# Performance work log

Measured on AMD Instinct MI355X. Metric: run time of the kernel, lower is better.

The kernel has to match this reference:

```python
import jax, jax.numpy as jnp
import numpy as np

HEAD_CHOICES = [8, 10, 12]
MAX_HEADS = 12
HEAD_DIM = 64
MAX_REL_POS = 14
SCALE = HEAD_DIM ** -0.5


def _rel_indices(N):
    # AutoFormer RelativePosition2D_super index computation (static, numpy).
    L = N - 1                      # remove cls token
    s = int(L ** 0.5)              # patches per row
    r = np.arange(L)
    dv = r[None, :] // s - r[:, None] // s
    dh = r[None, :] % s - r[:, None] % s
    iv = np.clip(dv, -MAX_REL_POS, MAX_REL_POS) + MAX_REL_POS + 1
    ih = np.clip(dh, -MAX_REL_POS, MAX_REL_POS) + MAX_REL_POS + 1
    iv = np.pad(iv, ((1, 0), (1, 0)))  # cls token row/col -> index 0
    ih = np.pad(ih, ((1, 0), (1, 0)))
    return jnp.asarray(iv), jnp.asarray(ih)


def setup_inputs() -> dict:
    key = jax.random.key(0)
    ks = jax.random.split(key, 6)
    B, N = 16, 577
    T = 2 * MAX_REL_POS + 2  # 30
    x = jax.random.normal(ks[0], (B, N, 3 * MAX_HEADS * HEAD_DIM), dtype=jnp.float32)
    weights = jax.nn.softmax(jax.random.normal(ks[1], (len(HEAD_CHOICES),), dtype=jnp.float32))
    rel_k_table_v = jax.random.normal(ks[2], (T, HEAD_DIM), dtype=jnp.float32) * 0.02
    rel_k_table_h = jax.random.normal(ks[3], (T, HEAD_DIM), dtype=jnp.float32) * 0.02
    rel_v_table_v = jax.random.normal(ks[4], (T, HEAD_DIM), dtype=jnp.float32) * 0.02
    rel_v_table_h = jax.random.normal(ks[5], (T, HEAD_DIM), dtype=jnp.float32) * 0.02
    return dict(x=x, weights=weights,
                rel_k_table_v=rel_k_table_v, rel_k_table_h=rel_k_table_h,
                rel_v_table_v=rel_v_table_v, rel_v_table_h=rel_v_table_h)


def reference(x, weights, rel_k_table_v, rel_k_table_h, rel_v_table_v, rel_v_table_h):
    B, N, _ = x.shape
    # [3, B, H, N, D]
    qkv = x.reshape(B, N, 3, MAX_HEADS, HEAD_DIM).transpose(2, 0, 3, 1, 4)
    # Mixture over head-count choices: slicing first c heads, scaling by w[i],
    # padding to max_heads, and summing == per-head weight sum_i w[i]*[h < c_i].
    head_mask = jnp.asarray(np.array([[1.0 if h < c else 0.0 for h in range(MAX_HEADS)]
                                      for c in HEAD_CHOICES]), dtype=x.dtype)  # [C, H]
    w_head = weights @ head_mask  # [H]
    w4 = w_head[None, :, None, None]
    q = qkv[0] * w4
    k = qkv[1] * w4
    v = qkv[2] * w4
    # content attention + relative-position K bias
    attn = jnp.einsum('bhnd,bhmd->bhnm', q, k) * SCALE
    iv, ih = _rel_indices(N)
    rel_k = rel_k_table_v[iv] + rel_k_table_h[ih]  # [N, N, D]
    attn = attn + jnp.einsum('bhnd,nmd->bhnm', q, rel_k) * SCALE
    attn = jax.nn.softmax(attn, axis=-1)  # attn_drop has p=0 (eval)
    out = jnp.einsum('bhnm,bhmd->bhnd', attn, v)
    rel_v = rel_v_table_v[iv] + rel_v_table_h[ih]  # [N, N, D]
    out = out + jnp.einsum('bhnm,nmd->bhnd', attn, rel_v)
    return out.transpose(0, 2, 1, 3).reshape(B, N, MAX_HEADS * HEAD_DIM)
```

## Files before the change

kernel.cpp:

```cpp
#include <hip/hip_runtime.h>

typedef short bf16x8_t __attribute__((ext_vector_type(8)));
typedef float f32x4_t __attribute__((ext_vector_type(4)));

#define NTOK 577
#define QPAD 640
#define MPAD 608
#define NSTEP 19

__device__ __forceinline__ unsigned short f2bf(float f) {
  unsigned u = __builtin_bit_cast(unsigned, f);
  u += 0x7FFFu + ((u >> 16) & 1u);
  return (unsigned short)(u >> 16);
}
__device__ __forceinline__ float headw(const float* wts, int h) {
  float w0 = wts[0], w1 = wts[1], w2 = wts[2];
  return (h < 8) ? (w0 + w1 + w2) : ((h < 10) ? (w1 + w2) : w2);
}
__device__ __forceinline__ unsigned rangemask(int lo, int hi) {
  lo = lo < 0 ? 0 : lo; hi = hi > 32 ? 32 : hi;
  if (hi <= lo) return 0u;
  unsigned mh = (hi >= 32) ? 0xFFFFFFFFu : ((1u << hi) - 1u);
  unsigned ml = (1u << lo) - 1u;
  return mh & ~ml;
}

extern "C" __global__ __launch_bounds__(256) void prep_x(
    const float* __restrict__ x, const float* __restrict__ wts,
    unsigned short* __restrict__ qbf, unsigned short* __restrict__ kbf,
    unsigned short* __restrict__ vbf) {
  __shared__ unsigned short t_s[64][72];
  const int tid = threadIdx.x;
  const int n0 = blockIdx.x * 64, h = blockIdx.y, b = blockIdx.z;
  const float w = headw(wts, h);
  const float qs = w * w * 0.125f;
  const float* xb = x + (size_t)(b * NTOK) * 2304 + h * 64;
  unsigned short* qo = qbf + ((size_t)(b * 12 + h)) * QPAD * 64;
  unsigned short* ko = kbf + ((size_t)(b * 12 + h)) * QPAD * 64;
  for (int p = 0; p < 4; ++p) {
    int idx = p * 256 + tid;
    int row = idx >> 4, c4 = idx & 15;
    int n = n0 + row;
    float4 vq = {0,0,0,0}, vk = {0,0,0,0}, vv = {0,0,0,0};
    if (n < NTOK) {
      const float* rp = xb + (size_t)n * 2304 + c4 * 4;
      vq = *(const float4*)rp;
      vk = *(const float4*)(rp + 768);
      vv = *(const float4*)(rp + 1536);
    }
    ushort4 oq, ok;
    oq.x = f2bf(vq.x * qs); oq.y = f2bf(vq.y * qs); oq.z = f2bf(vq.z * qs); oq.w = f2bf(vq.w * qs);
    ok.x = f2bf(vk.x); ok.y = f2bf(vk.y); ok.z = f2bf(vk.z); ok.w = f2bf(vk.w);
    *(ushort4*)(qo + (size_t)(n0 + row) * 64 + c4 * 4) = oq;
    *(ushort4*)(ko + (size_t)(n0 + row) * 64 + c4 * 4) = ok;
    t_s[c4 * 4 + 0][row] = f2bf(vv.x);
    t_s[c4 * 4 + 1][row] = f2bf(vv.y);
    t_s[c4 * 4 + 2][row] = f2bf(vv.z);
    t_s[c4 * 4 + 3][row] = f2bf(vv.w);
  }
  __syncthreads();
  for (int p = 0; p < 2; ++p) {
    int c = p * 256 + tid;
    int d = c >> 3, n8 = c & 7;
    bf16x8_t val = *(const bf16x8_t*)&t_s[d][n8 * 8];
    *(bf16x8_t*)(vbf + ((size_t)(b * 12 + h) * 64 + d) * QPAD + n0 + n8 * 8) = val;
  }
}

extern "C" __global__ __launch_bounds__(256) void prep_tab(
    const float* __restrict__ wts,
    const float* __restrict__ tkv, const float* __restrict__ tkh,
    const float* __restrict__ tvv, const float* __restrict__ tvh,
    unsigned short* __restrict__ tkb, unsigned short* __restrict__ tvb) {
  int tid = threadIdx.x, bx = blockIdx.x;
  if (bx < 48) {
    int cid = bx * 256 + tid;
    int d4 = cid & 15, t = (cid >> 4) & 31, tb = (cid >> 9) & 1, h = cid >> 10;
    float s = 1.f / headw(wts, h);
    const float* src = tb ? tkh : tkv;
    float4 v = {0,0,0,0};
    if (t < 30) v = *(const float4*)(src + t * 64 + d4 * 4);
    ushort4 o;
    o.x = f2bf(v.x * s); o.y = f2bf(v.y * s); o.z = f2bf(v.z * s); o.w = f2bf(v.w * s);
    *(ushort4*)(tkb + (((size_t)(h * 2 + tb)) * 32 + t) * 64 + d4 * 4) = o;
  } else {
    for (int i = 0; i < 16; ++i) {
      int id = tid * 16 + i;
      int t = id & 31, d = (id >> 5) & 63, tb = id >> 11;
      const float* src = tb ? tvh : tvv;
      tvb[id] = (t < 30) ? f2bf(src[t * 64 + d]) : (unsigned short)0;
    }
  }
}

struct __align__(16) SMem {
  float qg_s[2][64][25];
  unsigned gmask_s[2][NSTEP][25];
  float l_s[64];
  union {
    struct { float qv_t[2][64][30]; } pro;
    struct {
      unsigned short k_s[32][72];
      unsigned short v_sT[64][40];
      unsigned short P_s[64][40];
    } loop;
    struct { float sv_f[2][64][30]; } epi;
  } u;
};

extern "C" __global__ __launch_bounds__(256, 5) void hma_kernel(
    const unsigned short* __restrict__ qbf, const unsigned short* __restrict__ kbf,
    const unsigned short* __restrict__ vbf, const unsigned short* __restrict__ tkb,
    const unsigned short* __restrict__ tvb, const float* __restrict__ wts,
    float* __restrict__ out) {
  __shared__ SMem sm;
  const int tid = threadIdx.x;
  const int wave = tid >> 6, lane = tid & 63, quad = lane >> 4, l15 = lane & 15;
  const int rg = wave & 1;
  const int cg = wave >> 1;
  const int tb_w = cg;
  const int n0 = blockIdx.x * 64;
  const int h = blockIdx.y, b = blockIdx.z;
  const float w = headw(wts, h);

  const unsigned short* qb = qbf + ((size_t)(b * 12 + h)) * QPAD * 64;
  const unsigned short* kb = kbf + ((size_t)(b * 12 + h)) * QPAD * 64;
  const unsigned short* vb = vbf + ((size_t)(b * 12 + h)) * 64 * QPAD;

  bf16x8_t qa[2][2];
  for (int sub = 0; sub < 2; ++sub)
    for (int kk = 0; kk < 2; ++kk)
      qa[sub][kk] = *(const bf16x8_t*)(qb + (size_t)(n0 + rg * 32 + sub * 16 + l15) * 64 + kk * 32 + quad * 8);

  for (int p = tid; p < 2 * NSTEP * 25; p += 256) {
    int tb = p / (NSTEP * 25), r2 = p % (NSTEP * 25), step = r2 / 25, g = r2 % 25;
    int m0 = step * 32;
    unsigned mask;
    if (g == 24) {
      mask = rangemask(NTOK - m0, MPAD - m0);
      if (step == 0) mask |= 1u;
    } else if (tb == 0) {
      mask = rangemask(24 * g + 1 - m0, 24 * g + 25 - m0);
    } else {
      mask = 0u;
      int j0 = (g + 1 - m0) % 24; if (j0 < 0) j0 += 24;
      for (int j = j0; j < 32; j += 24) {
        int m = m0 + j;
        if (m >= 1 && m < NTOK) mask |= (1u << j);
      }
    }
    sm.gmask_s[tb][step][g] = mask;
  }

  {
    const unsigned short* tkp = tkb + ((size_t)(h * 2 + tb_w)) * 32 * 64;
    for (int tt = 0; tt < 2; ++tt) {
      for (int sub = 0; sub < 2; ++sub) {
        f32x4_t acc = {0.f, 0.f, 0.f, 0.f};
        for (int kk = 0; kk < 2; ++kk) {
          bf16x8_t bb = *(const bf16x8_t*)(tkp + (size_t)(tt * 16 + l15) * 64 + kk * 32 + quad * 8);
          acc = __builtin_amdgcn_mfma_f32_16x16x32_bf16(qa[sub][kk], bb, acc, 0, 0, 0);
        }
        int t = tt * 16 + l15;
        if (t < 30)
          for (int r = 0; r < 4; ++r)
            sm.u.pro.qv_t[tb_w][rg * 32 + sub * 16 + quad * 4 + r][t] = acc[r];
      }
    }
  }
  __syncthreads();
  for (int p = tid; p < 2 * 64 * 25; p += 256) {
    int tb = p / 1600, r2 = p % 1600, n = r2 / 25, g = r2 % 25;
    int n_g = n0 + n;
    int t;
    if (n_g == 0 || n_g >= NTOK || g == 24) t = 0;
    else {
      int base = tb ? ((n_g - 1) % 24) : ((n_g - 1) / 24);
      int dq = g - base; dq = dq < -14 ? -14 : (dq > 14 ? 14 : dq);
      t = dq + 15;
    }
    sm.qg_s[tb][n][g] = sm.u.pro.qv_t[tb][n][t];
  }

  const int m_loc = cg * 16 + l15;
  int rmv, cmv;
  if (m_loc == 0) { rmv = 0; cmv = -1; }
  else { rmv = (m_loc - 1) / 24; cmv = (m_loc - 1) - rmv * 24; }
  const bool cls_lane = (m_loc == 0);

  f32x4_t oacc[2][2] = {{{0,0,0,0},{0,0,0,0}},{{0,0,0,0},{0,0,0,0}}};
  f32x4_t rsacc[2][2] = {{{0,0,0,0},{0,0,0,0}},{{0,0,0,0},{0,0,0,0}}};

  const int krow = tid >> 3, kch = tid & 7;
  const int vrow = tid >> 2, vch = tid & 3;
  const unsigned short* kptr = kb + (size_t)krow * 64 + kch * 8;
  const unsigned short* vptr = vb + (size_t)vrow * QPAD + vch * 8;
  bf16x8_t kreg = *(const bf16x8_t*)kptr;
  bf16x8_t vreg = *(const bf16x8_t*)vptr;

  for (int step = 0; step < NSTEP; ++step) {
    const int m0 = step * 32;
    __syncthreads();
    *(bf16x8_t*)&sm.u.loop.k_s[krow][kch * 8] = kreg;
    *(bf16x8_t*)&sm.u.loop.v_sT[vrow][vch * 8] = vreg;
    __syncthreads();
    kreg = *(const bf16x8_t*)(kptr + (size_t)(m0 + 32) * 64);
    vreg = *(const bf16x8_t*)(vptr + (m0 + 32));
    f32x4_t s[2] = {{0,0,0,0},{0,0,0,0}};
    {
      bf16x8_t kb0 = *(const bf16x8_t*)&sm.u.loop.k_s[cg * 16 + l15][quad * 8];
      bf16x8_t kb1 = *(const bf16x8_t*)&sm.u.loop.k_s[cg * 16 + l15][32 + quad * 8];
      for (int sub = 0; sub < 2; ++sub) {
        s[sub] = __builtin_amdgcn_mfma_f32_16x16x32_bf16(qa[sub][0], kb0, s[sub], 0, 0, 0);
        s[sub] = __builtin_amdgcn_mfma_f32_16x16x32_bf16(qa[sub][1], kb1, s[sub], 0, 0, 0);
      }
    }
    const int m_g = m0 + m_loc;
    int ur = rmv, uc = cmv;
    if (cls_lane && step == 0) { ur = 24; uc = 24; }
    const bool mpad = (m_g >= NTOK);
    for (int sub = 0; sub < 2; ++sub)
      for (int r = 0; r < 4; ++r) {
        int n_loc = rg * 32 + sub * 16 + quad * 4 + r;
        float logit = s[sub][r] + sm.qg_s[0][n_loc][ur] + sm.qg_s[1][n_loc][uc];
        float p = __expf(logit);
        if (mpad) p = 0.f;
        unsigned u = __builtin_bit_cast(unsigned, p);
        sm.u.loop.P_s[n_loc][m_loc] = (unsigned short)((u + 0x8000u) >> 16);
      }
    { int c = cmv + 8; int carry = (c >= 24); cmv = carry ? c - 24 : c; rmv += 1 + carry; }
    __syncthreads();
    bf16x8_t pa[2];
    for (int sub = 0; sub < 2; ++sub)
      pa[sub] = *(const bf16x8_t*)&sm.u.loop.P_s[rg * 32 + sub * 16 + l15][quad * 8];
    for (int ds = 0; ds < 2; ++ds) {
      bf16x8_t bb = *(const bf16x8_t*)&sm.u.loop.v_sT[cg * 32 + ds * 16 + l15][quad * 8];
      for (int sub = 0; sub < 2; ++sub)
        oacc[sub][ds] = __builtin_amdgcn_mfma_f32_16x16x32_bf16(pa[sub], bb, oacc[sub][ds], 0, 0, 0);
    }
    for (int gt = 0; gt < 2; ++gt) {
      unsigned g = (unsigned)(gt * 16 + l15);
      unsigned mask = (g < 25) ? sm.gmask_s[tb_w][step][g] : 0u;
      unsigned bits = (mask >> (quad * 8)) & 0xFFu;
      unsigned y0 = ((bits & 0xFu) * 0x204081u) & 0x01010101u;
      unsigned y1 = ((bits >> 4) * 0x204081u) & 0x01010101u;
      unsigned p01 = y0 & 0x0101u, p23 = (y0 >> 16) & 0x0101u;
      unsigned p45 = y1 & 0x0101u, p67 = (y1 >> 16) & 0x0101u;
      union { unsigned uu[4]; bf16x8_t v; } gbu;
      gbu.uu[0] = ((p01 | (p01 << 8)) & 0x00010001u) * 0x3F80u;
      gbu.uu[1] = ((p23 | (p23 << 8)) & 0x00010001u) * 0x3F80u;
      gbu.uu[2] = ((p45 | (p45 << 8)) & 0x00010001u) * 0x3F80u;
      gbu.uu[3] = ((p67 | (p67 << 8)) & 0x00010001u) * 0x3F80u;
      for (int sub = 0; sub < 2; ++sub)
        rsacc[sub][gt] = __builtin_amdgcn_mfma_f32_16x16x32_bf16(pa[sub], gbu.v, rsacc[sub][gt], 0, 0, 0);
    }
  }

  __syncthreads();
  for (int e = tid; e < 2 * 64 * 30; e += 256) (&sm.u.epi.sv_f[0][0][0])[e] = 0.f;
  __syncthreads();
  for (int sub = 0; sub < 2; ++sub)
    for (int gt = 0; gt < 2; ++gt) {
      int g = gt * 16 + l15;
      if (g < 25) {
        for (int r = 0; r < 4; ++r) {
          int n_loc = rg * 32 + sub * 16 + quad * 4 + r;
          int n_g = n0 + n_loc;
          int t;
          if (n_g == 0 || n_g >= NTOK || g == 24) t = 0;
          else {
            int base = tb_w ? ((n_g - 1) % 24) : ((n_g - 1) / 24);
            int dq = g - base; dq = dq < -14 ? -14 : (dq > 14 ? 14 : dq);
            t = dq + 15;
          }
          atomicAdd(&sm.u.epi.sv_f[tb_w][n_loc][t], rsacc[sub][gt][r]);
        }
      }
    }
  __syncthreads();
  if (tid < 64) {
    float l = 0.f;
    for (int t = 0; t < 30; ++t) l += sm.u.epi.sv_f[0][tid][t];
    sm.l_s[tid] = l;
  }
  for (int sub = 0; sub < 2; ++sub)
    for (int ds = 0; ds < 2; ++ds)
      for (int r = 0; r < 4; ++r) oacc[sub][ds][r] *= w;
  for (int tb = 0; tb < 2; ++tb) {
    bf16x8_t av[2];
    for (int sub = 0; sub < 2; ++sub) {
      int n_loc = rg * 32 + sub * 16 + l15;
      for (int j = 0; j < 8; ++j) {
        int t = quad * 8 + j;
        float f = (t < 30) ? sm.u.epi.sv_f[tb][n_loc][t] : 0.f;
        unsigned u = __builtin_bit_cast(unsigned, f);
        av[sub][j] = (short)((u + 0x8000u) >> 16);
      }
    }
    for (int ds = 0; ds < 2; ++ds) {
      bf16x8_t bb = *(const bf16x8_t*)(tvb + ((size_t)(tb * 64 + cg * 32 + ds * 16 + l15)) * 32 + quad * 8);
      for (int sub = 0; sub < 2; ++sub)
        oacc[sub][ds] = __builtin_amdgcn_mfma_f32_16x16x32_bf16(av[sub], bb, oacc[sub][ds], 0, 0, 0);
    }
  }
  __syncthreads();
  float* ob = out + (size_t)b * NTOK * 768 + h * 64;
  for (int sub = 0; sub < 2; ++sub)
    for (int r = 0; r < 4; ++r) {
      int n_loc = rg * 32 + sub * 16 + quad * 4 + r;
      int n_g = n0 + n_loc;
      if (n_g < NTOK) {
        float inv = 1.f / sm.l_s[n_loc];
        for (int ds = 0; ds < 2; ++ds) {
          int d = cg * 32 + ds * 16 + l15;
          ob[(size_t)n_g * 768 + d] = oacc[sub][ds][r] * inv;
        }
      }
    }
}

extern "C" void kernel_launch(void* const* d_in, const int* in_sizes, int n_in,
                              void* d_out, int out_size, void* d_ws, size_t ws_size,
                              hipStream_t stream) {
  const float* x   = (const float*)d_in[0];
  const float* wts = (const float*)d_in[1];
  const float* tkv = (const float*)d_in[2];
  const float* tkh = (const float*)d_in[3];
  const float* tvv = (const float*)d_in[4];
  const float* tvh = (const float*)d_in[5];
  float* out = (float*)d_out;
  const int B = in_sizes[0] / (NTOK * 2304);

  unsigned short* ws = (unsigned short*)d_ws;
  size_t qkSz = (size_t)B * 12 * QPAD * 64;
  unsigned short* qbf = ws;
  unsigned short* kbf = ws + qkSz;
  unsigned short* vbf = ws + 2 * qkSz;
  unsigned short* tkb = vbf + qkSz;
  unsigned short* tvb = tkb + (size_t)12 * 2 * 32 * 64;

  prep_x<<<dim3(10, 12, B), 256, 0, stream>>>(x, wts, qbf, kbf, vbf);
  prep_tab<<<dim3(49, 1, 1), 256, 0, stream>>>(wts, tkv, tkh, tvv, tvh, tkb, tvb);
  hma_kernel<<<dim3(10, 12, B), 256, 0, stream>>>(qbf, kbf, vbf, tkb, tvb, wts, out);
}
```

Before: 274.9 us.

## Double-buffer K/V tiles and fold relative-position bias into MFMA via one-hot operands

K and V tiles are now double-buffered in shared memory, so each step writes the next tile while computing on the current one. This removes one of the two per-step barriers. The per-element LDS gathers of the q·rel_k bias (qg_s) are replaced by two extra MFMAs per sub-tile. These multiply bf16-packed qg rows by one-hot vectors built in registers, so the bias accumulates directly into the logits. The change trades extra MFMA work and some bf16 rounding of the bias for fewer LDS reads and barriers, and shared-memory use grows from the doubled buffers.

```diff
diff --git a/kernel.cpp b/kernel.cpp
--- a/kernel.cpp
+++ b/kernel.cpp
@@ -94,14 +94,13 @@
 }
 
 struct __align__(16) SMem {
-  float qg_s[2][64][25];
   unsigned gmask_s[2][NSTEP][25];
   float l_s[64];
-  union {
-    struct { float qv_t[2][64][30]; } pro;
+  union __align__(16) U {
+    struct { float qv_t[2][64][30]; float qg[2][64][25]; } pro;
     struct {
-      unsigned short k_s[32][72];
-      unsigned short v_sT[64][40];
+      unsigned short k_s[2][32][72];
+      unsigned short v_sT[2][64][40];
       unsigned short P_s[64][40];
     } loop;
     struct { float sv_f[2][64][30]; } epi;
@@ -126,6 +125,13 @@
   const unsigned short* qb = qbf + ((size_t)(b * 12 + h)) * QPAD * 64;
   const unsigned short* kb = kbf + ((size_t)(b * 12 + h)) * QPAD * 64;
   const unsigned short* vb = vbf + ((size_t)(b * 12 + h)) * 64 * QPAD;
+
+  const int krow = tid >> 3, kch = tid & 7;
+  const int vrow = tid >> 2, vch = tid & 3;
+  const unsigned short* kptr = kb + (size_t)krow * 64 + kch * 8;
+  const unsigned short* vptr = vb + (size_t)vrow * QPAD + vch * 8;
+  bf16x8_t kreg = *(const bf16x8_t*)kptr;
+  bf16x8_t vreg = *(const bf16x8_t*)vptr;
 
   bf16x8_t qa[2][2];
   for (int sub = 0; sub < 2; ++sub)
@@ -179,8 +185,25 @@
       int dq = g - base; dq = dq < -14 ? -14 : (dq > 14 ? 14 : dq);
       t = dq + 15;
     }
-    sm.qg_s[tb][n][g] = sm.u.pro.qv_t[tb][n][t];
-  }
+    sm.u.pro.qg[tb][n][g] = sm.u.pro.qv_t[tb][n][t];
+  }
+  __syncthreads();
+  bf16x8_t qga[2][2];
+  for (int sub = 0; sub < 2; ++sub)
+    for (int tb = 0; tb < 2; ++tb) {
+      int n_loc = rg * 32 + sub * 16 + l15;
+      for (int j = 0; j < 8; ++j) {
+        int g = quad * 8 + j;
+        float f = (g < 25) ? sm.u.pro.qg[tb][n_loc][g] : 0.f;
+        qga[sub][tb][j] = (short)f2bf(f);
+      }
+    }
+  __syncthreads();
+  *(bf16x8_t*)&sm.u.loop.k_s[0][krow][kch * 8] = kreg;
+  *(bf16x8_t*)&sm.u.loop.v_sT[0][vrow][vch * 8] = vreg;
+  kreg = *(const bf16x8_t*)(kptr + (size_t)32 * 64);
+  vreg = *(const bf16x8_t*)(vptr + 32);
+  __syncthreads();
 
   const int m_loc = cg * 16 + l15;
   int rmv, cmv;
@@ -191,39 +214,42 @@
   f32x4_t oacc[2][2] = {{{0,0,0,0},{0,0,0,0}},{{0,0,0,0},{0,0,0,0}}};
   f32x4_t rsacc[2][2] = {{{0,0,0,0},{0,0,0,0}},{{0,0,0,0},{0,0,0,0}}};
 
-  const int krow = tid >> 3, kch = tid & 7;
-  const int vrow = tid >> 2, vch = tid & 3;
-  const unsigned short* kptr = kb + (size_t)krow * 64 + kch * 8;
-  const unsigned short* vptr = vb + (size_t)vrow * QPAD + vch * 8;
-  bf16x8_t kreg = *(const bf16x8_t*)kptr;
-  bf16x8_t vreg = *(const bf16x8_t*)vptr;
-
+  int cur = 0;
   for (int step = 0; step < NSTEP; ++step) {
     const int m0 = step * 32;
-    __syncthreads();
-    *(bf16x8_t*)&sm.u.loop.k_s[krow][kch * 8] = kreg;
-    *(bf16x8_t*)&sm.u.loop.v_sT[vrow][vch * 8] = vreg;
-    __syncthreads();
-    kreg = *(const bf16x8_t*)(kptr + (size_t)(m0 + 32) * 64);
-    vreg = *(const bf16x8_t*)(vptr + (m0 + 32));
+    const int nxt = cur ^ 1;
+    int ur = rmv, uc = cmv;
+    if (cls_lane && step == 0) { ur = 24; uc = 24; }
+    unsigned tr = (unsigned)ur - (unsigned)(quad * 8);
+    unsigned tc = (unsigned)uc - (unsigned)(quad * 8);
+    union { unsigned uu[4]; bf16x8_t v; } gr, gc;
+#pragma unroll
+    for (int i = 0; i < 4; ++i) {
+      gr.uu[i] = ((tr >> 1) == (unsigned)i) ? (0x3F80u << (16 * (tr & 1))) : 0u;
+      gc.uu[i] = ((tc >> 1) == (unsigned)i) ? (0x3F80u << (16 * (tc & 1))) : 0u;
+    }
     f32x4_t s[2] = {{0,0,0,0},{0,0,0,0}};
     {
-      bf16x8_t kb0 = *(const bf16x8_t*)&sm.u.loop.k_s[cg * 16 + l15][quad * 8];
-      bf16x8_t kb1 = *(const bf16x8_t*)&sm.u.loop.k_s[cg * 16 + l15][32 + quad * 8];
+      bf16x8_t kb0 = *(const bf16x8_t*)&sm.u.loop.k_s[cur][m_loc][quad * 8];
+      bf16x8_t kb1 = *(const bf16x8_t*)&sm.u.loop.k_s[cur][m_loc][32 + quad * 8];
       for (int sub = 0; sub < 2; ++sub) {
         s[sub] = __builtin_amdgcn_mfma_f32_16x16x32_bf16(qa[sub][0], kb0, s[sub], 0, 0, 0);
         s[sub] = __builtin_amdgcn_mfma_f32_16x16x32_bf16(qa[sub][1], kb1, s[sub], 0, 0, 0);
-      }
-    }
-    const int m_g = m0 + m_loc;
-    int ur = rmv, uc = cmv;
-    if (cls_lane && step == 0) { ur = 24; uc = 24; }
-    const bool mpad = (m_g >= NTOK);
+        s[sub] = __builtin_amdgcn_mfma_f32_16x16x32_bf16(qga[sub][0], gr.v, s[sub], 0, 0, 0);
+        s[sub] = __builtin_amdgcn_mfma_f32_16x16x32_bf16(qga[sub][1], gc.v, s[sub], 0, 0, 0);
+      }
+    }
+    *(bf16x8_t*)&sm.u.loop.k_s[nxt][krow][kch * 8] = kreg;
+    *(bf16x8_t*)&sm.u.loop.v_sT[nxt][vrow][vch * 8] = vreg;
+    if (step < NSTEP - 2) {
+      kreg = *(const bf16x8_t*)(kptr + (size_t)(m0 + 64) * 64);
+      vreg = *(const bf16x8_t*)(vptr + (m0 + 64));
+    }
+    const bool mpad = (m0 + m_loc >= NTOK);
     for (int sub = 0; sub < 2; ++sub)
       for (int r = 0; r < 4; ++r) {
         int n_loc = rg * 32 + sub * 16 + quad * 4 + r;
-        float logit = s[sub][r] + sm.qg_s[0][n_loc][ur] + sm.qg_s[1][n_loc][uc];
-        float p = __expf(logit);
+        float p = __expf(s[sub][r]);
         if (mpad) p = 0.f;
         unsigned u = __builtin_bit_cast(unsigned, p);
         sm.u.loop.P_s[n_loc][m_loc] = (unsigned short)((u + 0x8000u) >> 16);
@@ -234,7 +260,7 @@
     for (int sub = 0; sub < 2; ++sub)
       pa[sub] = *(const bf16x8_t*)&sm.u.loop.P_s[rg * 32 + sub * 16 + l15][quad * 8];
     for (int ds = 0; ds < 2; ++ds) {
-      bf16x8_t bb = *(const bf16x8_t*)&sm.u.loop.v_sT[cg * 32 + ds * 16 + l15][quad * 8];
+      bf16x8_t bb = *(const bf16x8_t*)&sm.u.loop.v_sT[cur][cg * 32 + ds * 16 + l15][quad * 8];
       for (int sub = 0; sub < 2; ++sub)
         oacc[sub][ds] = __builtin_amdgcn_mfma_f32_16x16x32_bf16(pa[sub], bb, oacc[sub][ds], 0, 0, 0);
     }
@@ -254,9 +280,10 @@
       for (int sub = 0; sub < 2; ++sub)
         rsacc[sub][gt] = __builtin_amdgcn_mfma_f32_16x16x32_bf16(pa[sub], gbu.v, rsacc[sub][gt], 0, 0, 0);
     }
-  }
-
-  __syncthreads();
+    __syncthreads();
+    cur = nxt;
+  }
+
   for (int e = tid; e < 2 * 64 * 30; e += 256) (&sm.u.epi.sv_f[0][0][0])[e] = 0.f;
   __syncthreads();
   for (int sub = 0; sub < 2; ++sub)
```

Result: slower. 334.1 us (+21.5%).
